# Kernel tuning notes

Hardware: AMD Instinct MI355X
Metric: run time of the kernel (lower is better)

Reference implementation:

```python
import jax, jax.numpy as jnp
import numpy as np

N = 50000   # nodes
E = 800000  # edges
IN, H1, H2, OUT = 128, 256, 128, 1


def setup_inputs() -> dict:
    key = jax.random.key(0)
    ks = jax.random.split(key, 9)
    x = jax.random.normal(ks[0], (N, IN), dtype=jnp.float32)
    edge_index = jax.random.randint(ks[1], (2, E), 0, N, dtype=jnp.int32)
    def glorot(k, fan_in, fan_out):
        s = np.sqrt(6.0 / (fan_in + fan_out)).astype(np.float32)
        return jax.random.uniform(k, (fan_in, fan_out), jnp.float32, -s, s)
    W1 = glorot(ks[2], IN, H1)
    b1 = jnp.zeros((H1,), jnp.float32)
    W2 = glorot(ks[3], H1, H2)
    b2 = jnp.zeros((H2,), jnp.float32)
    W3 = glorot(ks[4], H2, OUT)
    b3 = jnp.zeros((OUT,), jnp.float32)
    return {"x": x, "edge_index": edge_index, "W1": W1, "b1": b1,
            "W2": W2, "b2": b2, "W3": W3, "b3": b3}


def _gcn_layer(x, W, b, src, dst, norm):
    # dense transform [N, d_in] @ [d_in, d_out]
    h = x @ W
    # degree-normalized sparse aggregation: out[dst] += norm * h[src]
    agg = jax.ops.segment_sum(h[src] * norm[:, None], dst, num_segments=N)
    return agg + b


def reference(x, edge_index, W1, b1, W2, b2, W3, b3):
    src, dst = edge_index[0], edge_index[1]
    # PyG GCNConv: add self loops, then symmetric normalization
    loop = jnp.arange(N, dtype=src.dtype)
    src = jnp.concatenate([src, loop])
    dst = jnp.concatenate([dst, loop])
    deg = jax.ops.segment_sum(jnp.ones_like(dst, jnp.float32), dst, num_segments=N)
    dis = jax.lax.rsqrt(jnp.maximum(deg, 1.0))  # deg >= 1 via self loops
    norm = dis[src] * dis[dst]  # [E+N]
    h1 = jax.nn.relu(_gcn_layer(x, W1, b1, src, dst, norm))
    h2 = jax.nn.relu(_gcn_layer(h1, W2, b2, src, dst, norm))
    y = _gcn_layer(h2, W3, b3, src, dst, norm).reshape(-1)
    return (y, h1, h2)
```

## Files before the change

### kernel.cpp

```cpp
#include <hip/hip_runtime.h>


typedef __attribute__((ext_vector_type(8))) short short8;
typedef __attribute__((ext_vector_type(4))) float f32x4;

static __device__ __forceinline__ unsigned short f2bf(float f){
  union { float f; unsigned u; } v; v.f = f;
  unsigned r = v.u + 0x7FFF + ((v.u >> 16) & 1);
  return (unsigned short)(r >> 16);
}
static __device__ __forceinline__ float2 bf2f2(unsigned u){
  union { unsigned u; float f; } a, b;
  a.u = u << 16; b.u = u & 0xffff0000u;
  return make_float2(a.f, b.f);
}

__global__ __launch_bounds__(256) void k_bin(
    const int* __restrict__ src, const int* __restrict__ dst,
    int* __restrict__ bcur, unsigned* __restrict__ pairs, int E){
  __shared__ int cl[256];
  int t = threadIdx.x;
  int e0 = blockIdx.x * 4096 + t;
  cl[t] = 0; __syncthreads();
  #pragma unroll
  for (int i = 0; i < 16; i++){
    int e = e0 + i*256;
    if (e < E) atomicAdd(&cl[dst[e] >> 8], 1);
  }
  __syncthreads();
  int c = cl[t];
  int g = (c > 0) ? atomicAdd(&bcur[t], c) : 0;
  cl[t] = g;
  __syncthreads();
  #pragma unroll
  for (int i = 0; i < 16; i++){
    int e = e0 + i*256;
    if (e < E){
      int d = dst[e];
      int b = d >> 8;
      int p = atomicAdd(&cl[b], 1);
      pairs[(b << 13) + p] = (unsigned)src[e] | ((unsigned)(d & 255) << 16);
    }
  }
}

__global__ __launch_bounds__(256) void k_place(
    const int* __restrict__ bcur, const unsigned* __restrict__ pairs,
    unsigned short* __restrict__ csr_src, int* __restrict__ rowptr,
    int* __restrict__ cnt, float* __restrict__ dis, int n, int nb){
  __shared__ int sh[256];
  __shared__ int ncnt[256];
  int t = threadIdx.x;
  int b = blockIdx.x;
  int v = (t < nb) ? bcur[t] : 0;
  sh[t] = v; __syncthreads();
  for (int off = 1; off < 256; off <<= 1){
    int x = (t >= off) ? sh[t-off] : 0;
    __syncthreads(); sh[t] += x; __syncthreads();
  }
  int csr_base = (b == 0) ? 0 : sh[b-1];
  int cnt_b = bcur[b];
  ncnt[t] = 0; __syncthreads();
  const unsigned* P = pairs + ((size_t)b << 13);
  for (int i = t; i < cnt_b; i += 256) atomicAdd(&ncnt[P[i] >> 16], 1);
  __syncthreads();
  int c = ncnt[t];
  sh[t] = c; __syncthreads();
  for (int off = 1; off < 256; off <<= 1){
    int x = (t >= off) ? sh[t-off] : 0;
    __syncthreads(); sh[t] += x; __syncthreads();
  }
  int noff = sh[t] - c;
  int node = (b << 8) + t;
  if (node < n){
    rowptr[node] = csr_base + noff;
    cnt[node] = c;
    dis[node] = rsqrtf((float)(c + 1));
  }
  ncnt[t] = noff; __syncthreads();
  for (int i = t; i < cnt_b; i += 256){
    unsigned u = P[i];
    int p = atomicAdd(&ncnt[u >> 16], 1);
    csr_src[csr_base + p] = (unsigned short)(u & 0xffff);
  }
}

__global__ void k_wprep(const float* __restrict__ W1, const float* __restrict__ W2,
                        unsigned short* __restrict__ Wf1, unsigned short* __restrict__ Wf2){
  int t = blockIdx.x*256 + threadIdx.x;
  if (t < 32768){
    int j = t & 7, lane = (t>>3) & 63, kt = (t>>9) & 3, nt = t >> 11;
    int nn = nt*16 + (lane & 15);
    int kk = kt*32 + (lane>>4)*8 + j;
    Wf1[t] = f2bf(W1[kk*256 + nn]);
  } else {
    int o = t - 32768;
    int j = o & 7, lane = (o>>3) & 63, nt = (o>>9) & 7, kt = o >> 12;
    int nn = nt*16 + (lane & 15);
    int kk = kt*32 + (lane>>4)*8 + j;
    Wf2[o] = f2bf(W2[kk*128 + nn]);
  }
}

__global__ void k_xbf16(const float4* __restrict__ x, uint2* __restrict__ xb, int nv){
  int i = blockIdx.x*256 + threadIdx.x;
  if (i < nv){
    float4 v = x[i];
    xb[i] = make_uint2((unsigned)f2bf(v.x) | ((unsigned)f2bf(v.y) << 16),
                       (unsigned)f2bf(v.z) | ((unsigned)f2bf(v.w) << 16));
  }
}

__global__ void k_aggL1(const unsigned* __restrict__ xb, unsigned* __restrict__ out,
                        const int* __restrict__ rowptr, const int* __restrict__ cnt,
                        const unsigned short* __restrict__ csr_src,
                        const float* __restrict__ dis, int n){
  int t = threadIdx.x;
  int lane = t & 63;
  int node = blockIdx.x*4 + (t >> 6);
  if (node >= n) return;
  float di = dis[node];
  float2 v = bf2f2(xb[(size_t)node*64 + lane]);
  float2 acc = make_float2(di*v.x, di*v.y);
  int start = rowptr[node];
  int mm = cnt[node];
  int j = 0;
  for (; j + 7 < mm; j += 8){
    int s[8]; unsigned uv[8]; float w[8];
    #pragma unroll
    for (int q = 0; q < 8; q++) s[q] = csr_src[start+j+q];
    #pragma unroll
    for (int q = 0; q < 8; q++){ w[q] = dis[s[q]]; uv[q] = xb[(size_t)s[q]*64 + lane]; }
    #pragma unroll
    for (int q = 0; q < 8; q++){
      float2 u = bf2f2(uv[q]);
      acc.x = fmaf(w[q], u.x, acc.x); acc.y = fmaf(w[q], u.y, acc.y);
    }
  }
  for (; j < mm; j++){
    int s = csr_src[start+j];
    float2 u = bf2f2(xb[(size_t)s*64 + lane]);
    float w = dis[s];
    acc.x = fmaf(w, u.x, acc.x); acc.y = fmaf(w, u.y, acc.y);
  }
  acc.x *= di; acc.y *= di;
  out[(size_t)node*64 + lane] =
      (unsigned)f2bf(acc.x) | ((unsigned)f2bf(acc.y) << 16);
}

__global__ void k_aggL2(const unsigned* __restrict__ t2b, float* __restrict__ h2,
                        const int* __restrict__ rowptr, const int* __restrict__ cnt,
                        const unsigned short* __restrict__ csr_src,
                        const float* __restrict__ dis,
                        const float* __restrict__ b2, const float* __restrict__ W3,
                        float* __restrict__ u, int n){
  int t = threadIdx.x;
  int lane = t & 63;
  int node = blockIdx.x*4 + (t >> 6);
  if (node >= n) return;
  float di = dis[node];
  float2 v = bf2f2(t2b[(size_t)node*64 + lane]);
  float2 acc = make_float2(di*v.x, di*v.y);
  int start = rowptr[node];
  int mm = cnt[node];
  int j = 0;
  for (; j + 7 < mm; j += 8){
    int s[8]; unsigned uv[8]; float w[8];
    #pragma unroll
    for (int q = 0; q < 8; q++) s[q] = csr_src[start+j+q];
    #pragma unroll
    for (int q = 0; q < 8; q++){ w[q] = dis[s[q]]; uv[q] = t2b[(size_t)s[q]*64 + lane]; }
    #pragma unroll
    for (int q = 0; q < 8; q++){
      float2 uu = bf2f2(uv[q]);
      acc.x = fmaf(w[q], uu.x, acc.x); acc.y = fmaf(w[q], uu.y, acc.y);
    }
  }
  for (; j < mm; j++){
    int s = csr_src[start+j];
    float2 uu = bf2f2(t2b[(size_t)s*64 + lane]);
    float w = dis[s];
    acc.x = fmaf(w, uu.x, acc.x); acc.y = fmaf(w, uu.y, acc.y);
  }
  float2 b = ((const float2*)b2)[lane];
  acc.x = fmaxf(fmaf(di, acc.x, b.x), 0.0f);
  acc.y = fmaxf(fmaf(di, acc.y, b.y), 0.0f);
  ((float2*)h2)[(size_t)node*64 + lane] = acc;
  float up = fmaf(acc.x, W3[2*lane], acc.y * W3[2*lane+1]);
  #pragma unroll
  for (int off = 32; off > 0; off >>= 1) up += __shfl_down(up, off);
  if (lane == 0) u[node] = up;
}

__global__ __launch_bounds__(256) void k_gemm1_mfma(
    const unsigned short* __restrict__ Xa, const unsigned short* __restrict__ Wf1,
    const float* __restrict__ bias, float* __restrict__ out, int n)
{
  __shared__ unsigned short Wl[8*4*64*8];
  __shared__ unsigned short As[64*136];
  int t = threadIdx.x;
  int row0 = (blockIdx.x >> 1) * 64;
  int h = blockIdx.x & 1;
  {
    const float4* src = (const float4*)Wf1 + (size_t)h*2048;
    float4* dst = (float4*)Wl;
    #pragma unroll
    for (int i = 0; i < 8; i++) dst[i*256 + t] = src[i*256 + t];
  }
  {
    const float4* src = (const float4*)Xa;
    #pragma unroll
    for (int i = 0; i < 4; i++){
      int f = i*256 + t, r = f >> 4, c = f & 15;
      float4 v = make_float4(0,0,0,0);
      if (row0 + r < n) v = src[(size_t)(row0+r)*16 + c];
      *(float4*)&As[r*136 + c*8] = v;
    }
  }
  __syncthreads();
  int w = t >> 6, lane = t & 63, m = lane & 15, q = lane >> 4;
  int rbase = w*16;
  short8 af[4];
  #pragma unroll
  for (int kt = 0; kt < 4; kt++)
    af[kt] = *(const short8*)&As[(rbase + m)*136 + kt*32 + q*8];
  f32x4 acc[8];
  #pragma unroll
  for (int i = 0; i < 8; i++) acc[i] = (f32x4){0.f,0.f,0.f,0.f};
  #pragma unroll
  for (int nt = 0; nt < 8; nt++){
    #pragma unroll
    for (int kt = 0; kt < 4; kt++){
      short8 bfr = *(const short8*)&Wl[((nt*4 + kt)*64 + lane)*8];
      acc[nt] = __builtin_amdgcn_mfma_f32_16x16x32_bf16(af[kt], bfr, acc[nt], 0, 0, 0);
    }
  }
  int rowa = row0 + rbase + q*4;
  int colb = h*128 + m;
  #pragma unroll
  for (int nt = 0; nt < 8; nt++){
    float b = bias[colb + nt*16];
    #pragma unroll
    for (int r = 0; r < 4; r++){
      int rr = rowa + r;
      if (rr < n) out[(size_t)rr*256 + colb + nt*16] = fmaxf(acc[nt][r] + b, 0.0f);
    }
  }
}

__global__ __launch_bounds__(256) void k_gemm2_mfma(
    const float* __restrict__ H1, const unsigned short* __restrict__ Wf2,
    unsigned short* __restrict__ T2b, int n)
{
  __shared__ unsigned short Wl[4*8*64*8];
  __shared__ unsigned short As[64*136];
  int t = threadIdx.x;
  int row0 = blockIdx.x * 64;
  int w = t >> 6, lane = t & 63, m = lane & 15, q = lane >> 4;
  int rbase = w*16;
  f32x4 acc[8];
  #pragma unroll
  for (int i = 0; i < 8; i++) acc[i] = (f32x4){0.f,0.f,0.f,0.f};
  for (int p = 0; p < 2; p++){
    if (p) __syncthreads();
    {
      const float4* src = (const float4*)Wf2 + (size_t)p*2048;
      float4* dst = (float4*)Wl;
      #pragma unroll
      for (int i = 0; i < 8; i++) dst[i*256 + t] = src[i*256 + t];
    }
    {
      #pragma unroll
      for (int i = 0; i < 8; i++){
        int f = i*256 + t;
        int r = f >> 5, c = f & 31;
        float4 v = make_float4(0,0,0,0);
        if (row0 + r < n) v = ((const float4*)H1)[(size_t)(row0+r)*64 + p*32 + c];
        unsigned lo = (unsigned)f2bf(v.x) | ((unsigned)f2bf(v.y) << 16);
        unsigned hi = (unsigned)f2bf(v.z) | ((unsigned)f2bf(v.w) << 16);
        *(uint2*)&As[r*136 + c*4] = make_uint2(lo, hi);
      }
    }
    __syncthreads();
    short8 af[4];
    #pragma unroll
    for (int kt = 0; kt < 4; kt++)
      af[kt] = *(const short8*)&As[(rbase + m)*136 + kt*32 + q*8];
    #pragma unroll
    for (int nt = 0; nt < 8; nt++){
      #pragma unroll
      for (int kt = 0; kt < 4; kt++){
        short8 bfr = *(const short8*)&Wl[((kt*8 + nt)*64 + lane)*8];
        acc[nt] = __builtin_amdgcn_mfma_f32_16x16x32_bf16(af[kt], bfr, acc[nt], 0, 0, 0);
      }
    }
  }
  int rowa = row0 + rbase + q*4;
  #pragma unroll
  for (int nt = 0; nt < 8; nt++){
    #pragma unroll
    for (int r = 0; r < 4; r++){
      int rr = rowa + r;
      if (rr < n) T2b[(size_t)rr*128 + nt*16 + m] = f2bf(acc[nt][r]);
    }
  }
}

__global__ void k_agg1d(const float* __restrict__ u, float* __restrict__ y,
                        const int* __restrict__ rowptr, const int* __restrict__ cnt,
                        const unsigned short* __restrict__ csr_src,
                        const float* __restrict__ dis,
                        const float* __restrict__ b3, int n){
  int i = blockIdx.x*256 + threadIdx.x;
  if (i >= n) return;
  float di = dis[i];
  float acc = di * u[i];
  int s0 = rowptr[i], m = cnt[i];
  for (int j = 0; j < m; j++){
    int s = csr_src[s0+j];
    acc = fmaf(dis[s], u[s], acc);
  }
  y[i] = fmaf(di, acc, b3[0]);
}

extern "C" void kernel_launch(void* const* d_in, const int* in_sizes, int n_in,
                              void* d_out, int out_size, void* d_ws, size_t ws_size,
                              hipStream_t stream){
  const float* x  = (const float*)d_in[0];
  const int*  ei  = (const int*)d_in[1];
  const float* W1 = (const float*)d_in[2];
  const float* b1 = (const float*)d_in[3];
  const float* W2 = (const float*)d_in[4];
  const float* b2 = (const float*)d_in[5];
  const float* W3 = (const float*)d_in[6];
  const float* b3 = (const float*)d_in[7];
  const int N = in_sizes[0] / 128;
  const int E = in_sizes[1] / 2;
  const int* src = ei;
  const int* dst = ei + E;
  const int NB = (N + 255) >> 8;

  char* p = (char*)d_ws;
  auto alloc = [&](size_t bytes)->char*{
    char* r = p; p += (bytes + 255) & ~(size_t)255; return r;
  };
  int*   bcur    = (int*)  alloc(256*4);
  int*   rowptr  = (int*)  alloc((size_t)N*4);
  int*   cnt     = (int*)  alloc((size_t)N*4);
  float* dis     = (float*)alloc((size_t)N*4);
  unsigned* pairs = (unsigned*)alloc((size_t)NB*8192*4);
  unsigned short* csr_src = (unsigned short*)alloc((size_t)E*2);
  unsigned* xb   = (unsigned*)alloc((size_t)N*128*2);
  unsigned* xa   = (unsigned*)alloc((size_t)N*128*2);
  unsigned short* t2b = (unsigned short*)alloc((size_t)N*128*2);
  float* u       = (float*)alloc((size_t)N*4);
  unsigned short* wf1 = (unsigned short*)alloc(32768*2);
  unsigned short* wf2 = (unsigned short*)alloc(32768*2);

  float* y  = (float*)d_out;
  float* h1 = y + N;
  float* h2 = h1 + (size_t)N*256;

  hipMemsetAsync(bcur, 0, 256*4, stream);
  int bb = (E + 4095)/4096;
  int nb = (N + 255)/256;
  k_bin   <<<bb, 256, 0, stream>>>(src, dst, bcur, pairs, E);
  k_place <<<NB, 256, 0, stream>>>(bcur, pairs, csr_src, rowptr, cnt, dis, N, NB);
  k_wprep <<<256, 256, 0, stream>>>(W1, W2, wf1, wf2);
  int xv = N*32;
  k_xbf16 <<<(xv+255)/256, 256, 0, stream>>>((const float4*)x, (uint2*)xb, xv);

  int ab = (N + 3)/4;
  int rb = (N + 63)/64;
  k_aggL1     <<<ab,   256, 0, stream>>>(xb, xa, rowptr, cnt, csr_src, dis, N);
  k_gemm1_mfma<<<rb*2, 256, 0, stream>>>((const unsigned short*)xa, wf1, b1, h1, N);
  k_gemm2_mfma<<<rb,   256, 0, stream>>>(h1, wf2, t2b, N);
  k_aggL2     <<<ab,   256, 0, stream>>>((const unsigned*)t2b, h2, rowptr, cnt, csr_src, dis, b2, W3, u, N);
  k_agg1d     <<<nb,   256, 0, stream>>>(u, y, rowptr, cnt, csr_src, dis, b3, N);
}
```

Measured before the change: 276.6 us.

## Merge prep kernels, widen aggregation unroll, feed GEMM2 from bf16 copy of h1

```diff
diff --git a/kernel.cpp b/kernel.cpp
--- a/kernel.cpp
+++ b/kernel.cpp
@@ -13,6 +13,37 @@
   union { unsigned u; float f; } a, b;
   a.u = u << 16; b.u = u & 0xffff0000u;
   return make_float2(a.f, b.f);
+}
+
+__global__ void k_prep(const float* __restrict__ W1, const float* __restrict__ W2,
+                       unsigned short* __restrict__ Wf1, unsigned short* __restrict__ Wf2,
+                       const float4* __restrict__ x, uint2* __restrict__ xb, int nv,
+                       int* __restrict__ bcur){
+  int blk = blockIdx.x;
+  int tid = threadIdx.x;
+  if (blk < 256){
+    if (blk == 0) bcur[tid] = 0;
+    int t = blk*256 + tid;
+    if (t < 32768){
+      int j = t & 7, lane = (t>>3) & 63, kt = (t>>9) & 3, nt = t >> 11;
+      int nn = nt*16 + (lane & 15);
+      int kk = kt*32 + (lane>>4)*8 + j;
+      Wf1[t] = f2bf(W1[kk*256 + nn]);
+    } else {
+      int o = t - 32768;
+      int j = o & 7, lane = (o>>3) & 63, nt = (o>>9) & 7, kt = o >> 12;
+      int nn = nt*16 + (lane & 15);
+      int kk = kt*32 + (lane>>4)*8 + j;
+      Wf2[o] = f2bf(W2[kk*128 + nn]);
+    }
+  } else {
+    int i = (blk - 256)*256 + tid;
+    if (i < nv){
+      float4 v = x[i];
+      xb[i] = make_uint2((unsigned)f2bf(v.x) | ((unsigned)f2bf(v.y) << 16),
+                         (unsigned)f2bf(v.z) | ((unsigned)f2bf(v.w) << 16));
+    }
+  }
 }
 
 __global__ __launch_bounds__(256) void k_bin(
@@ -85,32 +116,6 @@
   }
 }
 
-__global__ void k_wprep(const float* __restrict__ W1, const float* __restrict__ W2,
-                        unsigned short* __restrict__ Wf1, unsigned short* __restrict__ Wf2){
-  int t = blockIdx.x*256 + threadIdx.x;
-  if (t < 32768){
-    int j = t & 7, lane = (t>>3) & 63, kt = (t>>9) & 3, nt = t >> 11;
-    int nn = nt*16 + (lane & 15);
-    int kk = kt*32 + (lane>>4)*8 + j;
-    Wf1[t] = f2bf(W1[kk*256 + nn]);
-  } else {
-    int o = t - 32768;
-    int j = o & 7, lane = (o>>3) & 63, nt = (o>>9) & 7, kt = o >> 12;
-    int nn = nt*16 + (lane & 15);
-    int kk = kt*32 + (lane>>4)*8 + j;
-    Wf2[o] = f2bf(W2[kk*128 + nn]);
-  }
-}
-
-__global__ void k_xbf16(const float4* __restrict__ x, uint2* __restrict__ xb, int nv){
-  int i = blockIdx.x*256 + threadIdx.x;
-  if (i < nv){
-    float4 v = x[i];
-    xb[i] = make_uint2((unsigned)f2bf(v.x) | ((unsigned)f2bf(v.y) << 16),
-                       (unsigned)f2bf(v.z) | ((unsigned)f2bf(v.w) << 16));
-  }
-}
-
 __global__ void k_aggL1(const unsigned* __restrict__ xb, unsigned* __restrict__ out,
                         const int* __restrict__ rowptr, const int* __restrict__ cnt,
                         const unsigned short* __restrict__ csr_src,
@@ -125,14 +130,26 @@
   int start = rowptr[node];
   int mm = cnt[node];
   int j = 0;
-  for (; j + 7 < mm; j += 8){
-    int s[8]; unsigned uv[8]; float w[8];
-    #pragma unroll
-    for (int q = 0; q < 8; q++) s[q] = csr_src[start+j+q];
-    #pragma unroll
-    for (int q = 0; q < 8; q++){ w[q] = dis[s[q]]; uv[q] = xb[(size_t)s[q]*64 + lane]; }
-    #pragma unroll
-    for (int q = 0; q < 8; q++){
+  for (; j + 15 < mm; j += 16){
+    int s[16]; unsigned uv[16]; float w[16];
+    #pragma unroll
+    for (int q = 0; q < 16; q++) s[q] = csr_src[start+j+q];
+    #pragma unroll
+    for (int q = 0; q < 16; q++){ w[q] = dis[s[q]]; uv[q] = xb[(size_t)s[q]*64 + lane]; }
+    #pragma unroll
+    for (int q = 0; q < 16; q++){
+      float2 u = bf2f2(uv[q]);
+      acc.x = fmaf(w[q], u.x, acc.x); acc.y = fmaf(w[q], u.y, acc.y);
+    }
+  }
+  for (; j + 3 < mm; j += 4){
+    int s[4]; unsigned uv[4]; float w[4];
+    #pragma unroll
+    for (int q = 0; q < 4; q++) s[q] = csr_src[start+j+q];
+    #pragma unroll
+    for (int q = 0; q < 4; q++){ w[q] = dis[s[q]]; uv[q] = xb[(size_t)s[q]*64 + lane]; }
+    #pragma unroll
+    for (int q = 0; q < 4; q++){
       float2 u = bf2f2(uv[q]);
       acc.x = fmaf(w[q], u.x, acc.x); acc.y = fmaf(w[q], u.y, acc.y);
     }
@@ -164,14 +181,26 @@
   int start = rowptr[node];
   int mm = cnt[node];
   int j = 0;
-  for (; j + 7 < mm; j += 8){
-    int s[8]; unsigned uv[8]; float w[8];
-    #pragma unroll
-    for (int q = 0; q < 8; q++) s[q] = csr_src[start+j+q];
-    #pragma unroll
-    for (int q = 0; q < 8; q++){ w[q] = dis[s[q]]; uv[q] = t2b[(size_t)s[q]*64 + lane]; }
-    #pragma unroll
-    for (int q = 0; q < 8; q++){
+  for (; j + 15 < mm; j += 16){
+    int s[16]; unsigned uv[16]; float w[16];
+    #pragma unroll
+    for (int q = 0; q < 16; q++) s[q] = csr_src[start+j+q];
+    #pragma unroll
+    for (int q = 0; q < 16; q++){ w[q] = dis[s[q]]; uv[q] = t2b[(size_t)s[q]*64 + lane]; }
+    #pragma unroll
+    for (int q = 0; q < 16; q++){
+      float2 uu = bf2f2(uv[q]);
+      acc.x = fmaf(w[q], uu.x, acc.x); acc.y = fmaf(w[q], uu.y, acc.y);
+    }
+  }
+  for (; j + 3 < mm; j += 4){
+    int s[4]; unsigned uv[4]; float w[4];
+    #pragma unroll
+    for (int q = 0; q < 4; q++) s[q] = csr_src[start+j+q];
+    #pragma unroll
+    for (int q = 0; q < 4; q++){ w[q] = dis[s[q]]; uv[q] = t2b[(size_t)s[q]*64 + lane]; }
+    #pragma unroll
+    for (int q = 0; q < 4; q++){
       float2 uu = bf2f2(uv[q]);
       acc.x = fmaf(w[q], uu.x, acc.x); acc.y = fmaf(w[q], uu.y, acc.y);
     }
@@ -194,7 +223,8 @@
 
 __global__ __launch_bounds__(256) void k_gemm1_mfma(
     const unsigned short* __restrict__ Xa, const unsigned short* __restrict__ Wf1,
-    const float* __restrict__ bias, float* __restrict__ out, int n)
+    const float* __restrict__ bias, float* __restrict__ out,
+    unsigned short* __restrict__ h1b, int n)
 {
   __shared__ unsigned short Wl[8*4*64*8];
   __shared__ unsigned short As[64*136];
@@ -243,13 +273,17 @@
     #pragma unroll
     for (int r = 0; r < 4; r++){
       int rr = rowa + r;
-      if (rr < n) out[(size_t)rr*256 + colb + nt*16] = fmaxf(acc[nt][r] + b, 0.0f);
+      if (rr < n){
+        float o = fmaxf(acc[nt][r] + b, 0.0f);
+        out[(size_t)rr*256 + colb + nt*16] = o;
+        h1b[(size_t)rr*256 + colb + nt*16] = f2bf(o);
+      }
     }
   }
 }
 
 __global__ __launch_bounds__(256) void k_gemm2_mfma(
-    const float* __restrict__ H1, const unsigned short* __restrict__ Wf2,
+    const unsigned short* __restrict__ H1b, const unsigned short* __restrict__ Wf2,
     unsigned short* __restrict__ T2b, int n)
 {
   __shared__ unsigned short Wl[4*8*64*8];
@@ -270,15 +304,13 @@
       for (int i = 0; i < 8; i++) dst[i*256 + t] = src[i*256 + t];
     }
     {
+      const float4* src = (const float4*)H1b;
       #pragma unroll
-      for (int i = 0; i < 8; i++){
-        int f = i*256 + t;
-        int r = f >> 5, c = f & 31;
+      for (int i = 0; i < 4; i++){
+        int f = i*256 + t, r = f >> 4, c = f & 15;
         float4 v = make_float4(0,0,0,0);
-        if (row0 + r < n) v = ((const float4*)H1)[(size_t)(row0+r)*64 + p*32 + c];
-        unsigned lo = (unsigned)f2bf(v.x) | ((unsigned)f2bf(v.y) << 16);
-        unsigned hi = (unsigned)f2bf(v.z) | ((unsigned)f2bf(v.w) << 16);
-        *(uint2*)&As[r*136 + c*4] = make_uint2(lo, hi);
+        if (row0 + r < n) v = src[(size_t)(row0+r)*32 + p*16 + c];
+        *(float4*)&As[r*136 + c*8] = v;
       }
     }
     __syncthreads();
@@ -352,6 +384,7 @@
   unsigned short* csr_src = (unsigned short*)alloc((size_t)E*2);
   unsigned* xb   = (unsigned*)alloc((size_t)N*128*2);
   unsigned* xa   = (unsigned*)alloc((size_t)N*128*2);
+  unsigned short* h1b = (unsigned short*)alloc((size_t)N*256*2);
   unsigned short* t2b = (unsigned short*)alloc((size_t)N*128*2);
   float* u       = (float*)alloc((size_t)N*4);
   unsigned short* wf1 = (unsigned short*)alloc(32768*2);
@@ -361,20 +394,19 @@
   float* h1 = y + N;
   float* h2 = h1 + (size_t)N*256;
 
-  hipMemsetAsync(bcur, 0, 256*4, stream);
   int bb = (E + 4095)/4096;
   int nb = (N + 255)/256;
+  int xv = N*32;
+  k_prep  <<<256 + (xv+255)/256, 256, 0, stream>>>(W1, W2, wf1, wf2,
+                                                   (const float4*)x, (uint2*)xb, xv, bcur);
   k_bin   <<<bb, 256, 0, stream>>>(src, dst, bcur, pairs, E);
   k_place <<<NB, 256, 0, stream>>>(bcur, pairs, csr_src, rowptr, cnt, dis, N, NB);
-  k_wprep <<<256, 256, 0, stream>>>(W1, W2, wf1, wf2);
-  int xv = N*32;
-  k_xbf16 <<<(xv+255)/256, 256, 0, stream>>>((const float4*)x, (uint2*)xb, xv);
 
   int ab = (N + 3)/4;
   int rb = (N + 63)/64;
   k_aggL1     <<<ab,   256, 0, stream>>>(xb, xa, rowptr, cnt, csr_src, dis, N);
-  k_gemm1_mfma<<<rb*2, 256, 0, stream>>>((const unsigned short*)xa, wf1, b1, h1, N);
-  k_gemm2_mfma<<<rb,   256, 0, stream>>>(h1, wf2, t2b, N);
+  k_gemm1_mfma<<<rb*2, 256, 0, stream>>>((const unsigned short*)xa, wf1, b1, h1, h1b, N);
+  k_gemm2_mfma<<<rb,   256, 0, stream>>>(h1b, wf2, t2b, N);
   k_aggL2     <<<ab,   256, 0, stream>>>((const unsigned*)t2b, h2, rowptr, cnt, csr_src, dis, b2, W3, u, N);
   k_agg1d     <<<nb,   256, 0, stream>>>(u, y, rowptr, cnt, csr_src, dis, b3, N);
 }
```

Result: faster. 264.0 us (-4.6%).
